# Kernel tuning notes

Hardware: AMD Instinct MI355X
Metric: run time of the kernel (lower is better)

## Reference

```python
import jax, jax.numpy as jnp
import numpy as np

N, E, C_IN, C_OUT, NHEADS = 100000, 1600000, 128, 128, 4


def setup_inputs() -> dict:
    key = jax.random.key(0)
    k1, k2, k3, k4 = jax.random.split(key, 4)
    x = jax.random.normal(k1, (N, C_IN), dtype=jnp.float32)
    edge_index = jax.random.randint(k2, (2, E), 0, N, dtype=jnp.int32)
    batch_slices_x = jnp.array([0, N], dtype=jnp.int32)
    # glorot-style init scale
    weight = jax.random.normal(k3, (C_IN, C_OUT), dtype=jnp.float32) * (1.0 / np.sqrt(C_IN))
    att_weight = jax.random.normal(k4, (1, NHEADS, 2 * (C_OUT // NHEADS)), dtype=jnp.float32) * 0.1
    return {"x": x, "edge_index": edge_index, "batch_slices_x": batch_slices_x,
            "weight": weight, "att_weight": att_weight}


def reference(x, edge_index, batch_slices_x, weight, att_weight):
    # Eval-mode VotePoolLayer: hard attention via per-source-node argmax (scatter_max),
    # cat head-combine, no bias, att_act = identity, then graph pruning (relabel=False).
    n = x.shape[0]
    nheads = att_weight.shape[1]
    c1h = att_weight.shape[2] // 2  # out_channels per head

    h = (x @ weight).reshape(n, nheads, c1h)  # (N, H, c)
    w_j = att_weight[0, :, :c1h]              # (H, c) weights for source (x_j)
    w_i = att_weight[0, :, c1h:]              # (H, c) weights for target (x_i)
    # alpha[e,h] = sum_c h[src[e],h,c]*w_j[h,c] + h[dst[e],h,c]*w_i[h,c]
    s_j = jnp.einsum('nhc,hc->nh', h, w_j)    # (N, H)
    s_i = jnp.einsum('nhc,hc->nh', h, w_i)    # (N, H)

    src, dst = edge_index[0], edge_index[1]
    alpha = s_j[src] + s_i[dst]               # (E, H)

    # scatter_max argmax over edges grouped by src, per head -> one-hot alpha
    e = alpha.shape[0]
    seg_max = jax.ops.segment_max(alpha, src, num_segments=n)  # (N, H)
    is_max = alpha == seg_max[src]                             # (E, H)
    eids = jnp.arange(e, dtype=jnp.int32)[:, None]             # (E, 1)
    cand = jnp.where(is_max, eids, jnp.int32(e))
    seg_argmax = jax.ops.segment_min(cand, src, num_segments=n)  # (N, H) edge ids
    alpha_1hot = (eids == seg_argmax[src]).astype(h.dtype)       # (E, H)

    # message passing: weighted source features, scatter-add at destination
    msg = h[src] * alpha_1hot[:, :, None]                        # (E, H, c)
    out = jax.ops.segment_sum(msg, dst, num_segments=n)          # (N, H, c)
    out = out.reshape(n, nheads * c1h)                           # cat combine

    # edge selection (eval branch): alpha.sum(dim=1) > 0
    edge_select = alpha_1hot.sum(axis=1) > 0                     # (E,)

    # prune (relabel=False): nodes = unique(dst[edge_select]); keep edges with both
    # endpoints in node set; zero out features of the selected nodes.
    node_mask = jnp.zeros(n, dtype=jnp.int32).at[dst].max(edge_select.astype(jnp.int32)) > 0
    edge_keep = node_mask[src] & node_mask[dst]                  # (E,) subgraph edge mask
    x_out = jnp.where(node_mask[:, None], jnp.float32(0), out)

    return x_out, edge_keep, node_mask, batch_slices_x
```

## Files before the change

kernel.cpp:

```cpp
#include <hip/hip_runtime.h>
#include <stdint.h>

typedef unsigned long long u64;
typedef unsigned int u32;
typedef unsigned short u16;
typedef u32 u32x4 __attribute__((ext_vector_type(4)));
typedef float f32x4 __attribute__((ext_vector_type(4)));

#define CIN 128
#define NN 100000
#define EE 1600000

__device__ __forceinline__ float bf2f(u16 v) {
    union { u32 u; float f; } cv;
    cv.u = ((u32)v) << 16;
    return cv.f;
}

__device__ __forceinline__ u16 f2bf(float f) {
    u32 b = __float_as_uint(f);
    return (u16)((b + 0x7FFFu + ((b >> 16) & 1u)) >> 16);
}

__device__ __forceinline__ u32 mono32(float f) {
    u32 u = __float_as_uint(f);
    return ((int)u >= 0) ? (u | 0x80000000u) : ~u;
}

__global__ __launch_bounds__(256, 4) void k_s(const u16* __restrict__ x,
                                              const u16* __restrict__ W,
                                              const u16* __restrict__ att,
                                              ushort4* __restrict__ sjb,
                                              ushort4* __restrict__ sib,
                                              u32x4* __restrict__ xout16, int n_xout16,
                                              u32x4* __restrict__ seg16, int n_seg16,
                                              int* __restrict__ nm, int n_nodes) {
    int stride = gridDim.x * blockDim.x;
    int tid = blockIdx.x * blockDim.x + threadIdx.x;
    u32x4 z = { 0, 0, 0, 0 };
    for (int i = tid; i < n_xout16; i += stride) __builtin_nontemporal_store(z, &xout16[i]);
    for (int i = tid; i < n_seg16; i += stride) __builtin_nontemporal_store(z, &seg16[i]);
    for (int i = tid; i < n_nodes; i += stride) nm[i] = 0;

    __shared__ float Vl[1024];
    for (int slot = threadIdx.x; slot < 1024; slot += 256) {
        int k = slot >> 3, h8 = slot & 7;
        int head = h8 & 3;
        int off = (h8 < 4) ? 0 : 32;
        float acc = 0.0f;
        #pragma unroll
        for (int c = 0; c < 32; ++c)
            acc += bf2f(W[k * CIN + head * 32 + c]) * bf2f(att[head * 64 + off + c]);
        Vl[slot] = acc;
    }
    __syncthreads();

    for (int n = tid; n < n_nodes; n += stride) {
        const uint4* row = (const uint4*)(x + (size_t)n * CIN);
        float acc[8];
        #pragma unroll
        for (int h = 0; h < 8; ++h) acc[h] = 0.0f;
        #pragma unroll 4
        for (int q = 0; q < 16; ++q) {
            uint4 v = row[q];
            u32 w[4] = { v.x, v.y, v.z, v.w };
            #pragma unroll
            for (int j = 0; j < 4; ++j) {
                float x0 = bf2f((u16)(w[j] & 0xFFFFu));
                float x1 = bf2f((u16)(w[j] >> 16));
                int k0 = q * 8 + j * 2;
                #pragma unroll
                for (int h = 0; h < 8; ++h) acc[h] += x0 * Vl[k0 * 8 + h];
                #pragma unroll
                for (int h = 0; h < 8; ++h) acc[h] += x1 * Vl[(k0 + 1) * 8 + h];
            }
        }
        ushort4 a, b;
        a.x = f2bf(acc[0]); a.y = f2bf(acc[1]); a.z = f2bf(acc[2]); a.w = f2bf(acc[3]);
        b.x = f2bf(acc[4]); b.y = f2bf(acc[5]); b.z = f2bf(acc[6]); b.w = f2bf(acc[7]);
        sjb[n] = a;
        sib[n] = b;
    }
}

__global__ __launch_bounds__(256) void k_edge(const int* __restrict__ ei,
                                              const ushort4* __restrict__ sjb,
                                              const ushort4* __restrict__ sib,
                                              u64* __restrict__ seg, int n_edges) {
    int e = blockIdx.x * blockDim.x + threadIdx.x;
    if (e >= n_edges) return;
    int src = ei[e], dst = ei[n_edges + e];
    ushort4 sj = sjb[src];
    ushort4 si = sib[dst];
    u64 lo = (u64)(u32)(~(u32)e);
    u64* slot = seg + (size_t)src * 4;
    ulonglong2 c01 = *(const ulonglong2*)(slot);
    ulonglong2 c23 = *(const ulonglong2*)(slot + 2);
    u64 k0 = ((u64)mono32(bf2f(sj.x) + bf2f(si.x)) << 32) | lo;
    u64 k1 = ((u64)mono32(bf2f(sj.y) + bf2f(si.y)) << 32) | lo;
    u64 k2 = ((u64)mono32(bf2f(sj.z) + bf2f(si.z)) << 32) | lo;
    u64 k3 = ((u64)mono32(bf2f(sj.w) + bf2f(si.w)) << 32) | lo;
    if (k0 > c01.x) atomicMax(&slot[0], k0);
    if (k1 > c01.y) atomicMax(&slot[1], k1);
    if (k2 > c23.x) atomicMax(&slot[2], k2);
    if (k3 > c23.y) atomicMax(&slot[3], k3);
}

__global__ void k_select(const int* __restrict__ ei, const u64* __restrict__ seg,
                         int* __restrict__ nm, int n4, int n_edges) {
    int t = blockIdx.x * blockDim.x + threadIdx.x;
    if (t >= n4) return;
    u64 m = seg[t];
    if (m) {
        int e = (int)(~(u32)m);
        nm[ei[n_edges + e]] = 1;
    }
}

__global__ void k_final(const int* __restrict__ ei, const int* __restrict__ nm,
                        const int* __restrict__ slices, float* __restrict__ out,
                        int n_edges, int n_nodes, int ek_off, int nm_off, int sl_off) {
    int t = blockIdx.x * blockDim.x + threadIdx.x;
    int e0 = 4 * t;
    if (e0 < n_edges) {
        int4 srcs = ((const int4*)ei)[t];
        int4 dsts = ((const int4*)(ei + n_edges))[t];
        f32x4 v;
        v.x = (nm[srcs.x] & nm[dsts.x]) ? 1.0f : 0.0f;
        v.y = (nm[srcs.y] & nm[dsts.y]) ? 1.0f : 0.0f;
        v.z = (nm[srcs.z] & nm[dsts.z]) ? 1.0f : 0.0f;
        v.w = (nm[srcs.w] & nm[dsts.w]) ? 1.0f : 0.0f;
        __builtin_nontemporal_store(v, &((f32x4*)(out + ek_off))[t]);
    }
    if (t < n_nodes) out[nm_off + t] = nm[t] ? 1.0f : 0.0f;
    if (t < 2) out[sl_off + t] = (float)slices[t];
}

extern "C" void kernel_launch(void* const* d_in, const int* in_sizes, int n_in,
                              void* d_out, int out_size, void* d_ws, size_t ws_size,
                              hipStream_t stream) {
    const u16* x = nullptr; const int* ei = nullptr; const int* sl = nullptr;
    const u16* W = nullptr; const u16* att = nullptr;
    for (int i = 0; i < n_in; ++i) {
        switch (in_sizes[i]) {
            case NN * CIN:   x   = (const u16*)d_in[i]; break;
            case 2 * EE:     ei  = (const int*)d_in[i]; break;
            case 2:          sl  = (const int*)d_in[i]; break;
            case CIN * CIN:  W   = (const u16*)d_in[i]; break;
            case 256:        att = (const u16*)d_in[i]; break;
            default: break;
        }
    }
    if (!x || !ei || !sl || !W || !att) return;

    float* out = (float*)d_out;
    const int N = NN;
    const int E = EE;
    const int N4 = N * 4;

    const int ek_off = N * CIN;
    const int nm_off = ek_off + E;
    const int sl_off = nm_off + N;

    char* ws = (char*)d_ws;
    ushort4* sjb = (ushort4*)(ws);
    ushort4* sib = (ushort4*)(ws + (size_t)N * 8);
    int*     nm  = (int*)    (ws + (size_t)N * 16);
    u64*     seg = (u64*)    (ws + (size_t)N * 20);

    const int n_xout16 = N * CIN / 4;
    const int n_seg16  = N4 / 2;

    k_s<<<1280, 256, 0, stream>>>(x, W, att, sjb, sib,
                                  (u32x4*)out, n_xout16,
                                  (u32x4*)seg, n_seg16, nm, N);
    k_edge<<<(E + 255) / 256, 256, 0, stream>>>(ei, sjb, sib, seg, E);
    k_select<<<(N4 + 255) / 256, 256, 0, stream>>>(ei, seg, nm, N4, E);
    k_final<<<(E / 4 + 255) / 256, 256, 0, stream>>>(ei, nm, sl, out, E, N, ek_off, nm_off, sl_off);
}
```

Baseline: 204.1 us.

## Fuse four kernels into one persistent kernel with software grid barriers

```diff
diff --git a/kernel.cpp b/kernel.cpp
--- a/kernel.cpp
+++ b/kernel.cpp
@@ -10,6 +10,12 @@
 #define CIN 128
 #define NN 100000
 #define EE 1600000
+#define N4 (NN * 4)
+#define EK_OFF (NN * CIN)
+#define NM_OFF (EK_OFF + EE)
+#define SL_OFF (NM_OFF + NN)
+#define GRID 1024
+#define BLK 256
 
 __device__ __forceinline__ float bf2f(u16 v) {
     union { u32 u; float f; } cv;
@@ -27,23 +33,37 @@
     return ((int)u >= 0) ? (u | 0x80000000u) : ~u;
 }
 
-__global__ __launch_bounds__(256, 4) void k_s(const u16* __restrict__ x,
-                                              const u16* __restrict__ W,
-                                              const u16* __restrict__ att,
-                                              ushort4* __restrict__ sjb,
-                                              ushort4* __restrict__ sib,
-                                              u32x4* __restrict__ xout16, int n_xout16,
-                                              u32x4* __restrict__ seg16, int n_seg16,
-                                              int* __restrict__ nm, int n_nodes) {
-    int stride = gridDim.x * blockDim.x;
-    int tid = blockIdx.x * blockDim.x + threadIdx.x;
-    u32x4 z = { 0, 0, 0, 0 };
-    for (int i = tid; i < n_xout16; i += stride) __builtin_nontemporal_store(z, &xout16[i]);
-    for (int i = tid; i < n_seg16; i += stride) __builtin_nontemporal_store(z, &seg16[i]);
-    for (int i = tid; i < n_nodes; i += stride) nm[i] = 0;
+__device__ __forceinline__ void grid_barrier(u32* bar, u32 target) {
+    __syncthreads();
+    if (threadIdx.x == 0) {
+        __threadfence();
+        __hip_atomic_fetch_add(bar, 1u, __ATOMIC_ACQ_REL, __HIP_MEMORY_SCOPE_AGENT);
+        int spins = 0;
+        while (__hip_atomic_load(bar, __ATOMIC_RELAXED, __HIP_MEMORY_SCOPE_AGENT) < target) {
+            __builtin_amdgcn_s_sleep(8);
+            if (++spins > (1 << 22)) break;
+        }
+        __threadfence();
+    }
+    __syncthreads();
+}
+
+__global__ __launch_bounds__(256, 4) void k_fused(const u16* __restrict__ x,
+                                                  const int* __restrict__ ei,
+                                                  const int* __restrict__ sl,
+                                                  const u16* __restrict__ W,
+                                                  const u16* __restrict__ att,
+                                                  float* __restrict__ out,
+                                                  ushort4* __restrict__ sjb,
+                                                  ushort4* __restrict__ sib,
+                                                  int* __restrict__ nm,
+                                                  u64* __restrict__ seg,
+                                                  u32* __restrict__ bar) {
+    const int stride = GRID * BLK;
+    const int tid = blockIdx.x * BLK + threadIdx.x;
 
     __shared__ float Vl[1024];
-    for (int slot = threadIdx.x; slot < 1024; slot += 256) {
+    for (int slot = threadIdx.x; slot < 1024; slot += BLK) {
         int k = slot >> 3, h8 = slot & 7;
         int head = h8 & 3;
         int off = (h8 < 4) ? 0 : 32;
@@ -54,8 +74,7 @@
         Vl[slot] = acc;
     }
     __syncthreads();
-
-    for (int n = tid; n < n_nodes; n += stride) {
+    for (int n = tid; n < NN; n += stride) {
         const uint4* row = (const uint4*)(x + (size_t)n * CIN);
         float acc[8];
         #pragma unroll
@@ -81,59 +100,51 @@
         sjb[n] = a;
         sib[n] = b;
     }
-}
 
-__global__ __launch_bounds__(256) void k_edge(const int* __restrict__ ei,
-                                              const ushort4* __restrict__ sjb,
-                                              const ushort4* __restrict__ sib,
-                                              u64* __restrict__ seg, int n_edges) {
-    int e = blockIdx.x * blockDim.x + threadIdx.x;
-    if (e >= n_edges) return;
-    int src = ei[e], dst = ei[n_edges + e];
-    ushort4 sj = sjb[src];
-    ushort4 si = sib[dst];
-    u64 lo = (u64)(u32)(~(u32)e);
-    u64* slot = seg + (size_t)src * 4;
-    ulonglong2 c01 = *(const ulonglong2*)(slot);
-    ulonglong2 c23 = *(const ulonglong2*)(slot + 2);
-    u64 k0 = ((u64)mono32(bf2f(sj.x) + bf2f(si.x)) << 32) | lo;
-    u64 k1 = ((u64)mono32(bf2f(sj.y) + bf2f(si.y)) << 32) | lo;
-    u64 k2 = ((u64)mono32(bf2f(sj.z) + bf2f(si.z)) << 32) | lo;
-    u64 k3 = ((u64)mono32(bf2f(sj.w) + bf2f(si.w)) << 32) | lo;
-    if (k0 > c01.x) atomicMax(&slot[0], k0);
-    if (k1 > c01.y) atomicMax(&slot[1], k1);
-    if (k2 > c23.x) atomicMax(&slot[2], k2);
-    if (k3 > c23.y) atomicMax(&slot[3], k3);
-}
+    grid_barrier(bar, 1 * GRID);
 
-__global__ void k_select(const int* __restrict__ ei, const u64* __restrict__ seg,
-                         int* __restrict__ nm, int n4, int n_edges) {
-    int t = blockIdx.x * blockDim.x + threadIdx.x;
-    if (t >= n4) return;
-    u64 m = seg[t];
-    if (m) {
-        int e = (int)(~(u32)m);
-        nm[ei[n_edges + e]] = 1;
+    for (int e = tid; e < EE; e += stride) {
+        int src = ei[e], dst = ei[EE + e];
+        ushort4 sj = sjb[src];
+        ushort4 si = sib[dst];
+        u64 lo = (u64)(u32)(~(u32)e);
+        u64* slot = seg + (size_t)src * 4;
+        ulonglong2 c01 = *(const ulonglong2*)(slot);
+        ulonglong2 c23 = *(const ulonglong2*)(slot + 2);
+        u64 k0 = ((u64)mono32(bf2f(sj.x) + bf2f(si.x)) << 32) | lo;
+        u64 k1 = ((u64)mono32(bf2f(sj.y) + bf2f(si.y)) << 32) | lo;
+        u64 k2 = ((u64)mono32(bf2f(sj.z) + bf2f(si.z)) << 32) | lo;
+        u64 k3 = ((u64)mono32(bf2f(sj.w) + bf2f(si.w)) << 32) | lo;
+        if (k0 > c01.x) atomicMax(&slot[0], k0);
+        if (k1 > c01.y) atomicMax(&slot[1], k1);
+        if (k2 > c23.x) atomicMax(&slot[2], k2);
+        if (k3 > c23.y) atomicMax(&slot[3], k3);
     }
-}
 
-__global__ void k_final(const int* __restrict__ ei, const int* __restrict__ nm,
-                        const int* __restrict__ slices, float* __restrict__ out,
-                        int n_edges, int n_nodes, int ek_off, int nm_off, int sl_off) {
-    int t = blockIdx.x * blockDim.x + threadIdx.x;
-    int e0 = 4 * t;
-    if (e0 < n_edges) {
+    grid_barrier(bar, 2 * GRID);
+
+    for (int t = tid; t < N4; t += stride) {
+        u64 m = seg[t];
+        if (m) {
+            int e = (int)(~(u32)m);
+            nm[ei[EE + e]] = 1;
+        }
+    }
+
+    grid_barrier(bar, 3 * GRID);
+
+    for (int t = tid; t < EE / 4; t += stride) {
         int4 srcs = ((const int4*)ei)[t];
-        int4 dsts = ((const int4*)(ei + n_edges))[t];
+        int4 dsts = ((const int4*)(ei + EE))[t];
         f32x4 v;
         v.x = (nm[srcs.x] & nm[dsts.x]) ? 1.0f : 0.0f;
         v.y = (nm[srcs.y] & nm[dsts.y]) ? 1.0f : 0.0f;
         v.z = (nm[srcs.z] & nm[dsts.z]) ? 1.0f : 0.0f;
         v.w = (nm[srcs.w] & nm[dsts.w]) ? 1.0f : 0.0f;
-        __builtin_nontemporal_store(v, &((f32x4*)(out + ek_off))[t]);
+        __builtin_nontemporal_store(v, &((f32x4*)(out + EK_OFF))[t]);
     }
-    if (t < n_nodes) out[nm_off + t] = nm[t] ? 1.0f : 0.0f;
-    if (t < 2) out[sl_off + t] = (float)slices[t];
+    for (int t = tid; t < NN; t += stride) out[NM_OFF + t] = nm[t] ? 1.0f : 0.0f;
+    if (tid < 2) out[SL_OFF + tid] = (float)sl[tid];
 }
 
 extern "C" void kernel_launch(void* const* d_in, const int* in_sizes, int n_in,
@@ -154,27 +165,16 @@
     if (!x || !ei || !sl || !W || !att) return;
 
     float* out = (float*)d_out;
-    const int N = NN;
-    const int E = EE;
-    const int N4 = N * 4;
-
-    const int ek_off = N * CIN;
-    const int nm_off = ek_off + E;
-    const int sl_off = nm_off + N;
 
     char* ws = (char*)d_ws;
-    ushort4* sjb = (ushort4*)(ws);
-    ushort4* sib = (ushort4*)(ws + (size_t)N * 8);
-    int*     nm  = (int*)    (ws + (size_t)N * 16);
-    u64*     seg = (u64*)    (ws + (size_t)N * 20);
+    u32*     bar = (u32*)    (ws);
+    u64*     seg = (u64*)    (ws + 64);
+    int*     nm  = (int*)    (ws + 64 + (size_t)N4 * 8);
+    ushort4* sjb = (ushort4*)(ws + 64 + (size_t)N4 * 8 + (size_t)NN * 4);
+    ushort4* sib = (ushort4*)(ws + 64 + (size_t)N4 * 8 + (size_t)NN * 4 + (size_t)NN * 8);
 
-    const int n_xout16 = N * CIN / 4;
-    const int n_seg16  = N4 / 2;
+    hipMemsetAsync(ws, 0, 64 + (size_t)N4 * 8 + (size_t)NN * 4, stream);
+    hipMemsetAsync(out, 0, (size_t)EK_OFF * 4, stream);
 
-    k_s<<<1280, 256, 0, stream>>>(x, W, att, sjb, sib,
-                                  (u32x4*)out, n_xout16,
-                                  (u32x4*)seg, n_seg16, nm, N);
-    k_edge<<<(E + 255) / 256, 256, 0, stream>>>(ei, sjb, sib, seg, E);
-    k_select<<<(N4 + 255) / 256, 256, 0, stream>>>(ei, seg, nm, N4, E);
-    k_final<<<(E / 4 + 255) / 256, 256, 0, stream>>>(ei, nm, sl, out, E, N, ek_off, nm_off, sl_off);
+    k_fused<<<GRID, BLK, 0, stream>>>(x, ei, sl, W, att, out, sjb, sib, nm, seg, bar);
 }
```

Result: slower. 623.1 us (+205.2%).
